# Performance work log

Measured on AMD Instinct MI355X. Metric: run time of the kernel, lower is better.

The kernel has to match this reference:

```python
import jax, jax.numpy as jnp
import numpy as np

N_NODES = 32
N_EDGES = N_NODES * (N_NODES - 1)  # 992
BATCH = 16
SEQ = 8
BS = BATCH * SEQ  # 128 frames
D = 256  # node_latent_dim == edge_latent_dim
ITERS = 3


def gru_cell(x, h, Wih, Whh, bih, bhh):
    # torch GRUCell: gates ordered (r, z, n)
    gi = x @ Wih.T + bih
    gh = h @ Whh.T + bhh
    ir, iz, inn = jnp.split(gi, 3, axis=-1)
    hr, hz, hn = jnp.split(gh, 3, axis=-1)
    r = jax.nn.sigmoid(ir + hr)
    z = jax.nn.sigmoid(iz + hz)
    n = jnp.tanh(inn + r * hn)
    return (1.0 - z) * n + z * h


def setup_inputs() -> dict:
    key = jax.random.key(0)
    ks = jax.random.split(key, 16)
    s = 0.05
    inp = {
        'node_latents': jax.random.normal(ks[0], (BS * N_NODES, D), jnp.float32),
        'edge_latents': jax.random.normal(ks[1], (BS * N_EDGES, D), jnp.float32),
        'node_Wih': jax.random.normal(ks[2], (3 * D, D), jnp.float32) * s,
        'node_Whh': jax.random.normal(ks[3], (3 * D, D), jnp.float32) * s,
        'node_bih': jax.random.normal(ks[4], (3 * D,), jnp.float32) * s,
        'node_bhh': jax.random.normal(ks[5], (3 * D,), jnp.float32) * s,
        'edge_Wih': jax.random.normal(ks[6], (3 * D, D), jnp.float32) * s,
        'edge_Whh': jax.random.normal(ks[7], (3 * D, D), jnp.float32) * s,
        'edge_bih': jax.random.normal(ks[8], (3 * D,), jnp.float32) * s,
        'edge_bhh': jax.random.normal(ks[9], (3 * D,), jnp.float32) * s,
        'w_node_pool': jax.random.normal(ks[10], (2 * D,), jnp.float32) * s,
        'w_edge_pool_sub': jax.random.normal(ks[11], (2 * D,), jnp.float32) * s,
        'w_edge_pool_obj': jax.random.normal(ks[12], (2 * D,), jnp.float32) * s,
    }
    # all ordered (subject, object) pairs with subject != object, same for every frame
    pairs = np.array([(i, j) for i in range(N_NODES) for j in range(N_NODES) if i != j], dtype=np.int32)  # [E,2]
    e2n = np.concatenate([np.arange(N_EDGES, dtype=np.int32)[:, None], pairs], axis=1)  # [E,3]
    inp['edge_idx_to_node_idxs'] = jnp.asarray(np.broadcast_to(e2n, (BS, N_EDGES, 3)).copy())
    return inp


def reference(node_latents, edge_latents, node_Wih, node_Whh, node_bih, node_bhh,
              edge_Wih, edge_Whh, edge_bih, edge_bhh,
              w_node_pool, w_edge_pool_sub, w_edge_pool_obj, edge_idx_to_node_idxs):
    sub = edge_idx_to_node_idxs[..., 1].astype(jnp.int32)  # [BS,E]
    obj = edge_idx_to_node_idxs[..., 2].astype(jnp.int32)
    bidx = jnp.arange(BS, dtype=jnp.int32)[:, None]
    sub_flat = (bidx * N_NODES + sub).reshape(-1)  # [BS*E]
    obj_flat = (bidx * N_NODES + obj).reshape(-1)

    # initial GRU call with zero hidden state (torch GRUCell default)
    node_hidden = gru_cell(node_latents, jnp.zeros_like(node_latents), node_Wih, node_Whh, node_bih, node_bhh)
    edge_hidden = gru_cell(edge_latents, jnp.zeros_like(edge_latents), edge_Wih, edge_Whh, edge_bih, edge_bhh)

    for _ in range(ITERS):
        nh = node_hidden.reshape(BS, N_NODES, D)
        eh = edge_hidden.reshape(BS, N_EDGES, D)
        ns = jnp.take_along_axis(nh, sub[:, :, None], axis=1)  # [BS,E,D] subject node feats
        no = jnp.take_along_axis(nh, obj[:, :, None], axis=1)  # [BS,E,D]
        cat_s = jnp.concatenate([ns, eh], axis=-1)  # [BS,E,2D]
        cat_o = jnp.concatenate([no, eh], axis=-1)
        g_node = jax.nn.sigmoid(cat_s @ w_node_pool)[..., None]        # [BS,E,1]
        g_sub = jax.nn.sigmoid(cat_s @ w_edge_pool_sub)[..., None]
        g_obj = jax.nn.sigmoid(cat_o @ w_edge_pool_obj)[..., None]
        # node message: gated edge features scattered to subject and object nodes
        # (equivalent to the dense 0/1 incidence matmul since subject != object per edge)
        msg_e = (g_node * eh).reshape(-1, D)  # [BS*E,D]
        node_msg = (jax.ops.segment_sum(msg_e, sub_flat, num_segments=BS * N_NODES)
                    + jax.ops.segment_sum(msg_e, obj_flat, num_segments=BS * N_NODES))  # [BS*N,D]
        edge_msg = (g_sub * ns + g_obj * no).reshape(-1, D)  # [BS*E,D]
        node_hidden = gru_cell(node_msg, node_hidden, node_Wih, node_Whh, node_bih, node_bhh)
        edge_hidden = gru_cell(edge_msg, edge_hidden, edge_Wih, edge_Whh, edge_bih, edge_bhh)

    return (node_hidden.reshape(BS, N_NODES, D), edge_hidden.reshape(BS, N_EDGES, D))
```

## Files before the change

### kernel.cpp

```cpp
#include <hip/hip_runtime.h>


#define D_DIM 256
#define NNODE 32
#define NEDGE 992
#define EDGE_ROWS (128 * NEDGE)
#define NODE_ROWS (128 * NNODE)
#define BM 64
#define EGRID (EDGE_ROWS / BM)
#define NGRID (NODE_ROWS / BM)
#define GI_OFF 32768
#define GI_STR 776

typedef _Float16 half8 __attribute__((ext_vector_type(8)));
typedef _Float16 half4v __attribute__((ext_vector_type(4)));
typedef __attribute__((ext_vector_type(4))) float f32x4;

__device__ __forceinline__ float sigf(float x) { return 1.0f / (1.0f + __expf(-x)); }
__device__ __forceinline__ float tanh_fast(float x) { return 2.0f / (1.0f + __expf(-2.0f * x)) - 1.0f; }
__device__ __forceinline__ float dot4(float4 a, float4 b) { return a.x*b.x + a.y*b.y + a.z*b.z + a.w*b.w; }

__global__ __launch_bounds__(64) void pack_w(const float* __restrict__ Wih,
                                             const float* __restrict__ Whh,
                                             _Float16* __restrict__ ph) {
  const int ct = blockIdx.x;
  const int ks = blockIdx.y;
  const int l = threadIdx.x;
  const int col = ct * 16 + (l & 15);
  const int kb = ks * 32 + (l >> 4) * 8;
  const float* src = (kb < 256) ? (Wih + col * 256 + kb) : (Whh + col * 256 + (kb - 256));
  half8 v;
  #pragma unroll
  for (int j = 0; j < 8; ++j) v[j] = (_Float16)src[j];
  *(half8*)(ph + ((ct * 16 + ks) * 64 + l) * 8) = v;
}

__global__ __launch_bounds__(1024, 4) void gru_init(
    const float* __restrict__ xe, const float* __restrict__ xn,
    _Float16* __restrict__ eh16, float* __restrict__ hn,
    const _Float16* __restrict__ wpe, const _Float16* __restrict__ wpn,
    const float* __restrict__ ebih, const float* __restrict__ ebhh,
    const float* __restrict__ nbih, const float* __restrict__ nbhh) {
  __shared__ __align__(16) unsigned char lds[32768];
  const bool edge = blockIdx.x < EGRID;
  const int bx = edge ? blockIdx.x : (blockIdx.x - EGRID);
  const float* xsrc = edge ? xe : xn;
  const _Float16* wp = edge ? wpe : wpn;
  const float* bih = edge ? ebih : nbih;
  const float* bhh = edge ? ebhh : nbhh;

  const int t = threadIdx.x;
  const int rb = bx * BM;
  const int srow = t >> 4;
  const int skc = t & 15;
  const int w = t >> 6;
  const int l = t & 63;
  const int lq = l >> 4;
  const int lr = l & 15;
  const int swm = (lr & 7) << 4;
  const int swz = (srow & 7) << 4;
  const int rowg = rb + srow;

  #pragma unroll
  for (int c = 0; c < 2; ++c) {
    half8 hx;
    #pragma unroll
    for (int pq = 0; pq < 2; ++pq) {
      const float4 a = *(const float4*)(xsrc + rowg * D_DIM + c * 128 + skc * 8 + pq * 4);
      hx[pq * 4 + 0] = (_Float16)a.x; hx[pq * 4 + 1] = (_Float16)a.y;
      hx[pq * 4 + 2] = (_Float16)a.z; hx[pq * 4 + 3] = (_Float16)a.w;
    }
    *(half8*)(&lds[(srow * 512 + c * 256 + skc * 16) ^ swz]) = hx;
  }
  __syncthreads();

  const f32x4 zz = {0.f, 0.f, 0.f, 0.f};
  f32x4 acc_r[4] = {zz, zz, zz, zz};
  f32x4 acc_z[4] = {zz, zz, zz, zz};
  f32x4 acc_nx[4] = {zz, zz, zz, zz};

  #pragma unroll
  for (int ksg = 0; ksg < 8; ++ksg) {
    half8 ah[4];
    #pragma unroll
    for (int rf = 0; rf < 4; ++rf)
      ah[rf] = *(const half8*)(&lds[((rf * 16 + lr) * 512 + ksg * 64 + lq * 16) ^ swm]);
    const half8 br_ = *(const half8*)(wp + (((0 * 16 + w) * 16 + ksg) * 64 + l) * 8);
    const half8 bz_ = *(const half8*)(wp + (((1 * 16 + w) * 16 + ksg) * 64 + l) * 8);
    const half8 bn_ = *(const half8*)(wp + (((2 * 16 + w) * 16 + ksg) * 64 + l) * 8);
    #pragma unroll
    for (int rf = 0; rf < 4; ++rf)
      acc_r[rf] = __builtin_amdgcn_mfma_f32_16x16x32_f16(ah[rf], br_, acc_r[rf], 0, 0, 0);
    #pragma unroll
    for (int rf = 0; rf < 4; ++rf)
      acc_z[rf] = __builtin_amdgcn_mfma_f32_16x16x32_f16(ah[rf], bz_, acc_z[rf], 0, 0, 0);
    #pragma unroll
    for (int rf = 0; rf < 4; ++rf)
      acc_nx[rf] = __builtin_amdgcn_mfma_f32_16x16x32_f16(ah[rf], bn_, acc_nx[rf], 0, 0, 0);
  }

  const int col = w * 16 + lr;
  const float br = bih[col] + bhh[col];
  const float bz = bih[256 + col] + bhh[256 + col];
  const float bnx = bih[512 + col];
  const float bnh = bhh[512 + col];

  if (edge) {
    _Float16 sv[16];
    #pragma unroll
    for (int rf = 0; rf < 4; ++rf) {
      #pragma unroll
      for (int q = 0; q < 4; ++q) {
        const float r = sigf(acc_r[rf][q] + br);
        const float z = sigf(acc_z[rf][q] + bz);
        const float n = tanh_fast(acc_nx[rf][q] + bnx + r * bnh);
        sv[rf * 4 + q] = (_Float16)((1.0f - z) * n);
      }
    }
    __syncthreads();
    #pragma unroll
    for (int rf = 0; rf < 4; ++rf) {
      #pragma unroll
      for (int q = 0; q < 4; ++q) {
        const int rowl = rf * 16 + lq * 4 + q;
        *(_Float16*)(&lds[(rowl * 512 + col * 2) ^ ((rowl & 7) << 4)]) = sv[rf * 4 + q];
      }
    }
    __syncthreads();
    #pragma unroll
    for (int p = 0; p < 2; ++p) {
      const int c = t + p * 1024;
      const int row = c >> 5;
      const int kc = c & 31;
      *(uint4*)(eh16 + (rb + row) * 256 + kc * 8) =
          *(const uint4*)(&lds[(row * 512 + kc * 16) ^ ((row & 7) << 4)]);
    }
  } else {
    #pragma unroll
    for (int rf = 0; rf < 4; ++rf) {
      #pragma unroll
      for (int q = 0; q < 4; ++q) {
        const int rowl = rf * 16 + lq * 4 + q;
        const float r = sigf(acc_r[rf][q] + br);
        const float z = sigf(acc_z[rf][q] + bz);
        const float n = tanh_fast(acc_nx[rf][q] + bnx + r * bnh);
        hn[(rb + rowl) * D_DIM + col] = (1.0f - z) * n;
      }
    }
  }
}

__global__ __launch_bounds__(1024, 4) void gru_nw(
    const float* __restrict__ nh, const _Float16* __restrict__ wp,
    _Float16* __restrict__ nw,
    const float* __restrict__ wnp, const float* __restrict__ wes,
    const float* __restrict__ weo,
    float* __restrict__ dA, float* __restrict__ dS, float* __restrict__ dO) {
  __shared__ __align__(16) unsigned char lds[32768];
  const int t = threadIdx.x;
  const int rb = blockIdx.x * BM;
  const int srow = t >> 4;
  const int skc = t & 15;
  const int w = t >> 6;
  const int l = t & 63;
  const int lq = l >> 4;
  const int lr = l & 15;
  const int swm = (lr & 7) << 4;
  const int swz = (srow & 7) << 4;
  const int rowg = rb + srow;

  float4 xa[4];
  #pragma unroll
  for (int i = 0; i < 4; ++i)
    xa[i] = *(const float4*)(nh + rowg * D_DIM + (i >> 1) * 128 + skc * 8 + (i & 1) * 4);
  #pragma unroll
  for (int c = 0; c < 2; ++c) {
    half8 hx;
    const float* f0 = (const float*)&xa[c * 2];
    #pragma unroll
    for (int j = 0; j < 8; ++j) hx[j] = (_Float16)f0[j];
    *(half8*)(&lds[(srow * 512 + c * 256 + skc * 16) ^ swz]) = hx;
  }
  float p1 = 0.f, p2 = 0.f, p3 = 0.f;
  #pragma unroll
  for (int i = 0; i < 4; ++i) {
    const int k0 = (i >> 1) * 128 + skc * 8 + (i & 1) * 4;
    p1 += dot4(xa[i], *(const float4*)(wnp + k0));
    p2 += dot4(xa[i], *(const float4*)(wes + k0));
    p3 += dot4(xa[i], *(const float4*)(weo + k0));
  }
  #pragma unroll
  for (int mm = 1; mm < 16; mm <<= 1) {
    p1 += __shfl_xor(p1, mm, 16);
    p2 += __shfl_xor(p2, mm, 16);
    p3 += __shfl_xor(p3, mm, 16);
  }
  if (skc == 0) { dA[rowg] = p1; dS[rowg] = p2; dO[rowg] = p3; }
  __syncthreads();

  const f32x4 zz = {0.f, 0.f, 0.f, 0.f};
  f32x4 acc_r[4] = {zz, zz, zz, zz};
  f32x4 acc_z[4] = {zz, zz, zz, zz};
  f32x4 acc_nx[4] = {zz, zz, zz, zz};

  #pragma unroll
  for (int ksg = 0; ksg < 8; ++ksg) {
    half8 ah[4];
    #pragma unroll
    for (int rf = 0; rf < 4; ++rf)
      ah[rf] = *(const half8*)(&lds[((rf * 16 + lr) * 512 + ksg * 64 + lq * 16) ^ swm]);
    const half8 br_ = *(const half8*)(wp + (((0 * 16 + w) * 16 + ksg) * 64 + l) * 8);
    const half8 bz_ = *(const half8*)(wp + (((1 * 16 + w) * 16 + ksg) * 64 + l) * 8);
    const half8 bn_ = *(const half8*)(wp + (((2 * 16 + w) * 16 + ksg) * 64 + l) * 8);
    #pragma unroll
    for (int rf = 0; rf < 4; ++rf)
      acc_r[rf] = __builtin_amdgcn_mfma_f32_16x16x32_f16(ah[rf], br_, acc_r[rf], 0, 0, 0);
    #pragma unroll
    for (int rf = 0; rf < 4; ++rf)
      acc_z[rf] = __builtin_amdgcn_mfma_f32_16x16x32_f16(ah[rf], bz_, acc_z[rf], 0, 0, 0);
    #pragma unroll
    for (int rf = 0; rf < 4; ++rf)
      acc_nx[rf] = __builtin_amdgcn_mfma_f32_16x16x32_f16(ah[rf], bn_, acc_nx[rf], 0, 0, 0);
  }

  const int col = w * 16 + lr;
  #pragma unroll
  for (int rf = 0; rf < 4; ++rf) {
    #pragma unroll
    for (int q = 0; q < 4; ++q) {
      const int rowl = rf * 16 + lq * 4 + q;
      _Float16* np = nw + (rb + rowl) * 768 + col;
      np[0]   = (_Float16)acc_r[rf][q];
      np[256] = (_Float16)acc_z[rf][q];
      np[512] = (_Float16)acc_nx[rf][q];
    }
  }
}

template <bool LAST>
__global__ __launch_bounds__(1024, 4) void gru_iter(
    _Float16* __restrict__ eh16, float* __restrict__ ehf,
    float* __restrict__ nh, const float* __restrict__ nmsg,
    const _Float16* __restrict__ wpe, const _Float16* __restrict__ wpn,
    const float* __restrict__ ebih, const float* __restrict__ ebhh,
    const float* __restrict__ nbih, const float* __restrict__ nbhh,
    const float* __restrict__ wesb, const float* __restrict__ weob,
    const float* __restrict__ dotS, const float* __restrict__ dotO,
    const _Float16* __restrict__ nw) {
  __shared__ __align__(16) unsigned char lds[32768 + BM * GI_STR * 2];

  const int t = threadIdx.x;
  const int srow = t >> 4;
  const int skc = t & 15;
  const int w = t >> 6;
  const int l = t & 63;
  const int lq = l >> 4;
  const int lr = l & 15;
  const int swm = (lr & 7) << 4;
  const int swz = (srow & 7) << 4;

  const f32x4 zz = {0.f, 0.f, 0.f, 0.f};
  f32x4 acc_r[4] = {zz, zz, zz, zz};
  f32x4 acc_z[4] = {zz, zz, zz, zz};
  f32x4 acc_nx[4] = {zz, zz, zz, zz};
  f32x4 acc_nh[4] = {zz, zz, zz, zz};

  if (blockIdx.x < EGRID) {
    const int rb = blockIdx.x * BM;
    const int rowg = rb + srow;
    const int b = rowg / NEDGE;
    const int e = rowg - b * NEDGE;
    const int si = e / 31;
    const int m = e - si * 31;
    const int ob = (m < si) ? m : (m + 1);

    const uint4 v0 = *(const uint4*)(eh16 + rowg * 256 + skc * 8);
    const uint4 v1 = *(const uint4*)(eh16 + rowg * 256 + 128 + skc * 8);
    *(uint4*)(&lds[(srow * 512 + skc * 16) ^ swz]) = v0;
    *(uint4*)(&lds[(srow * 512 + 256 + skc * 16) ^ swz]) = v1;
    float pS = 0.f, pO = 0.f;
    {
      const _Float16* f0 = (const _Float16*)&v0;
      const _Float16* f1 = (const _Float16*)&v1;
      #pragma unroll
      for (int j = 0; j < 8; ++j) {
        const float a = (float)f0[j];
        const float bb = (float)f1[j];
        pS += a * wesb[skc * 8 + j] + bb * wesb[128 + skc * 8 + j];
        pO += a * weob[skc * 8 + j] + bb * weob[128 + skc * 8 + j];
      }
    }
    #pragma unroll
    for (int mm = 1; mm < 16; mm <<= 1) {
      pS += __shfl_xor(pS, mm, 16);
      pO += __shfl_xor(pO, mm, 16);
    }
    const float gs = sigf(dotS[b * NNODE + si] + pS);
    const float go = sigf(dotO[b * NNODE + ob] + pO);
    const _Float16 gsh = (_Float16)gs, goh = (_Float16)go;
    const _Float16* ns = nw + (b * NNODE + si) * 768;
    const _Float16* no_ = nw + (b * NNODE + ob) * 768;
    _Float16* giw = (_Float16*)(lds + GI_OFF) + srow * GI_STR;
    #pragma unroll
    for (int j = 0; j < 6; ++j) {
      const int c0 = skc * 8 + j * 128;
      const half8 a = *(const half8*)(ns + c0);
      const half8 bb = *(const half8*)(no_ + c0);
      half8 g;
      #pragma unroll
      for (int k = 0; k < 8; ++k) g[k] = gsh * a[k] + goh * bb[k];
      *(half8*)(giw + c0) = g;
    }
    __syncthreads();

    #pragma unroll
    for (int ksg = 0; ksg < 8; ++ksg) {
      half8 ah[4];
      #pragma unroll
      for (int rf = 0; rf < 4; ++rf)
        ah[rf] = *(const half8*)(&lds[((rf * 16 + lr) * 512 + ksg * 64 + lq * 16) ^ swm]);
      const int kk = 8 + ksg;
      const half8 br_ = *(const half8*)(wpe + (((0 * 16 + w) * 16 + kk) * 64 + l) * 8);
      const half8 bz_ = *(const half8*)(wpe + (((1 * 16 + w) * 16 + kk) * 64 + l) * 8);
      const half8 bn_ = *(const half8*)(wpe + (((2 * 16 + w) * 16 + kk) * 64 + l) * 8);
      #pragma unroll
      for (int rf = 0; rf < 4; ++rf)
        acc_r[rf] = __builtin_amdgcn_mfma_f32_16x16x32_f16(ah[rf], br_, acc_r[rf], 0, 0, 0);
      #pragma unroll
      for (int rf = 0; rf < 4; ++rf)
        acc_z[rf] = __builtin_amdgcn_mfma_f32_16x16x32_f16(ah[rf], bz_, acc_z[rf], 0, 0, 0);
      #pragma unroll
      for (int rf = 0; rf < 4; ++rf)
        acc_nh[rf] = __builtin_amdgcn_mfma_f32_16x16x32_f16(ah[rf], bn_, acc_nh[rf], 0, 0, 0);
    }

    const int col = w * 16 + lr;
    const float br = ebih[col] + ebhh[col];
    const float bz = ebih[256 + col] + ebhh[256 + col];
    const float bnx = ebih[512 + col];
    const float bnh = ebhh[512 + col];
    const _Float16* gir = (const _Float16*)(lds + GI_OFF);
    _Float16 sv[16];
    #pragma unroll
    for (int rf = 0; rf < 4; ++rf) {
      #pragma unroll
      for (int q = 0; q < 4; ++q) {
        const int rowl = rf * 16 + lq * 4 + q;
        const _Float16* gp = gir + rowl * GI_STR + col;
        const float r = sigf(acc_r[rf][q] + (float)gp[0] + br);
        const float z = sigf(acc_z[rf][q] + (float)gp[256] + bz);
        const float n = tanh_fast((float)gp[512] + bnx + r * (acc_nh[rf][q] + bnh));
        const float hv =
            (float)*(const _Float16*)(&lds[(rowl * 512 + col * 2) ^ ((rowl & 7) << 4)]);
        const float out = (1.0f - z) * n + z * hv;
        if constexpr (LAST) {
          ehf[(rb + rowl) * D_DIM + col] = out;
        } else {
          sv[rf * 4 + q] = (_Float16)out;
        }
      }
    }
    if constexpr (!LAST) {
      __syncthreads();
      #pragma unroll
      for (int rf = 0; rf < 4; ++rf) {
        #pragma unroll
        for (int q = 0; q < 4; ++q) {
          const int rowl = rf * 16 + lq * 4 + q;
          *(_Float16*)(&lds[(rowl * 512 + col * 2) ^ ((rowl & 7) << 4)]) = sv[rf * 4 + q];
        }
      }
      __syncthreads();
      #pragma unroll
      for (int p = 0; p < 2; ++p) {
        const int c = t + p * 1024;
        const int row = c >> 5;
        const int kc = c & 31;
        *(uint4*)(eh16 + (rb + row) * 256 + kc * 8) =
            *(const uint4*)(&lds[(row * 512 + kc * 16) ^ ((row & 7) << 4)]);
      }
    }
  } else {
    const int rb = (blockIdx.x - EGRID) * BM;
    const int rowg = rb + srow;

    {
      float4 pre[4];
      #pragma unroll
      for (int i = 0; i < 4; ++i)
        pre[i] = *(const float4*)(nh + rowg * D_DIM + (i >> 1) * 128 + skc * 8 + (i & 1) * 4);
      #pragma unroll
      for (int c = 0; c < 2; ++c) {
        half8 hh8;
        const float* f1 = (const float*)&pre[c * 2];
        #pragma unroll
        for (int j = 0; j < 8; ++j) hh8[j] = (_Float16)f1[j];
        *(half8*)(&lds[(srow * 1024 + 512 + c * 256 + skc * 16) ^ swz]) = hh8;
      }
    }
    __syncthreads();

    #pragma unroll
    for (int ksg = 0; ksg < 8; ++ksg) {
      half8 ah[4];
      #pragma unroll
      for (int rf = 0; rf < 4; ++rf)
        ah[rf] = *(const half8*)(&lds[((rf * 16 + lr) * 1024 + 512 + ksg * 64 + lq * 16) ^ swm]);
      const int kk = 8 + ksg;
      const half8 br_ = *(const half8*)(wpn + (((0 * 16 + w) * 16 + kk) * 64 + l) * 8);
      const half8 bz_ = *(const half8*)(wpn + (((1 * 16 + w) * 16 + kk) * 64 + l) * 8);
      const half8 bn_ = *(const half8*)(wpn + (((2 * 16 + w) * 16 + kk) * 64 + l) * 8);
      #pragma unroll
      for (int rf = 0; rf < 4; ++rf)
        acc_r[rf] = __builtin_amdgcn_mfma_f32_16x16x32_f16(ah[rf], br_, acc_r[rf], 0, 0, 0);
      #pragma unroll
      for (int rf = 0; rf < 4; ++rf)
        acc_z[rf] = __builtin_amdgcn_mfma_f32_16x16x32_f16(ah[rf], bz_, acc_z[rf], 0, 0, 0);
      #pragma unroll
      for (int rf = 0; rf < 4; ++rf)
        acc_nh[rf] = __builtin_amdgcn_mfma_f32_16x16x32_f16(ah[rf], bn_, acc_nh[rf], 0, 0, 0);
    }

    #pragma unroll
    for (int c = 0; c < 2; ++c) {
      half8 hx;
      #pragma unroll
      for (int pq = 0; pq < 2; ++pq) {
        const float4 a = *(const float4*)(nmsg + rowg * D_DIM + c * 128 + skc * 8 + pq * 4);
        hx[pq * 4 + 0] = (_Float16)a.x; hx[pq * 4 + 1] = (_Float16)a.y;
        hx[pq * 4 + 2] = (_Float16)a.z; hx[pq * 4 + 3] = (_Float16)a.w;
      }
      *(half8*)(&lds[(srow * 1024 + 0 + c * 256 + skc * 16) ^ swz]) = hx;
    }
    __syncthreads();
    #pragma unroll
    for (int ksg = 0; ksg < 8; ++ksg) {
      half8 ah[4];
      #pragma unroll
      for (int rf = 0; rf < 4; ++rf)
        ah[rf] = *(const half8*)(&lds[((rf * 16 + lr) * 1024 + 0 + ksg * 64 + lq * 16) ^ swm]);
      const half8 br_ = *(const half8*)(wpn + (((0 * 16 + w) * 16 + ksg) * 64 + l) * 8);
      const half8 bz_ = *(const half8*)(wpn + (((1 * 16 + w) * 16 + ksg) * 64 + l) * 8);
      const half8 bn_ = *(const half8*)(wpn + (((2 * 16 + w) * 16 + ksg) * 64 + l) * 8);
      #pragma unroll
      for (int rf = 0; rf < 4; ++rf)
        acc_r[rf] = __builtin_amdgcn_mfma_f32_16x16x32_f16(ah[rf], br_, acc_r[rf], 0, 0, 0);
      #pragma unroll
      for (int rf = 0; rf < 4; ++rf)
        acc_z[rf] = __builtin_amdgcn_mfma_f32_16x16x32_f16(ah[rf], bz_, acc_z[rf], 0, 0, 0);
      #pragma unroll
      for (int rf = 0; rf < 4; ++rf)
        acc_nx[rf] = __builtin_amdgcn_mfma_f32_16x16x32_f16(ah[rf], bn_, acc_nx[rf], 0, 0, 0);
    }

    const int col = w * 16 + lr;
    const float br = nbih[col] + nbhh[col];
    const float bz = nbih[256 + col] + nbhh[256 + col];
    const float bnx = nbih[512 + col];
    const float bnh = nbhh[512 + col];
    #pragma unroll
    for (int rf = 0; rf < 4; ++rf) {
      #pragma unroll
      for (int q = 0; q < 4; ++q) {
        const int rowl = rf * 16 + lq * 4 + q;
        const float r = sigf(acc_r[rf][q] + br);
        const float z = sigf(acc_z[rf][q] + bz);
        const float n = tanh_fast(acc_nx[rf][q] + bnx + r * (acc_nh[rf][q] + bnh));
        const float hv = nh[(rb + rowl) * D_DIM + col];
        nh[(rb + rowl) * D_DIM + col] = (1.0f - z) * n + z * hv;
      }
    }
  }
}

__global__ __launch_bounds__(256) void node_msg_kernel(
    const _Float16* __restrict__ eh16, const float* __restrict__ wnp,
    const float* __restrict__ dotA, float* __restrict__ nmsg) {
  __shared__ float sh[3][256];
  const int nr = blockIdx.x;
  const int b = nr >> 5;
  const int n = nr & 31;
  const int wv = threadIdx.x >> 6;
  const int l = threadIdx.x & 63;
  const int base = b * NEDGE;
  const float4 w1b = ((const float4*)(wnp + 256))[l];

  float4 acc = {0.f, 0.f, 0.f, 0.f};
  for (int k = wv; k < 62; k += 4) {
    int e, sub;
    if (k < 31) {
      e = base + n * 31 + k;
      sub = n;
    } else {
      int i = k - 31;
      const int ip = (i < n) ? i : (i + 1);
      e = base + ip * 31 + ((n < ip) ? n : (n - 1));
      sub = ip;
    }
    const half4v hv4 = ((const half4v*)(eh16 + e * 256))[l];
    float4 ev;
    ev.x = (float)hv4[0]; ev.y = (float)hv4[1];
    ev.z = (float)hv4[2]; ev.w = (float)hv4[3];
    float p = dot4(ev, w1b);
    #pragma unroll
    for (int mm = 32; mm > 0; mm >>= 1) p += __shfl_xor(p, mm, 64);
    const float gN = sigf(dotA[b * NNODE + sub] + p);
    acc.x += gN * ev.x; acc.y += gN * ev.y; acc.z += gN * ev.z; acc.w += gN * ev.w;
  }
  if (wv > 0) *(float4*)(&sh[wv - 1][l * 4]) = acc;
  __syncthreads();
  if (wv == 0) {
    #pragma unroll
    for (int v = 0; v < 3; ++v) {
      const float4 o = *(const float4*)(&sh[v][l * 4]);
      acc.x += o.x; acc.y += o.y; acc.z += o.z; acc.w += o.w;
    }
    *(float4*)(nmsg + nr * D_DIM + l * 4) = acc;
  }
}

extern "C" void kernel_launch(void* const* d_in, const int* in_sizes, int n_in,
                              void* d_out, int out_size, void* d_ws, size_t ws_size,
                              hipStream_t stream) {
  const float* node_latents = (const float*)d_in[0];
  const float* edge_latents = (const float*)d_in[1];
  const float* node_Wih = (const float*)d_in[2];
  const float* node_Whh = (const float*)d_in[3];
  const float* node_bih = (const float*)d_in[4];
  const float* node_bhh = (const float*)d_in[5];
  const float* edge_Wih = (const float*)d_in[6];
  const float* edge_Whh = (const float*)d_in[7];
  const float* edge_bih = (const float*)d_in[8];
  const float* edge_bhh = (const float*)d_in[9];
  const float* w_node_pool = (const float*)d_in[10];
  const float* w_edge_sub = (const float*)d_in[11];
  const float* w_edge_obj = (const float*)d_in[12];

  float* nh = (float*)d_out;
  float* eh = (float*)d_out + NODE_ROWS * D_DIM;

  const int WPLANE = 48 * 16 * 64 * 8;
  _Float16* ph_n = (_Float16*)d_ws;
  _Float16* ph_e = ph_n + WPLANE;
  _Float16* NW = ph_e + WPLANE;
  _Float16* eh16 = NW + NODE_ROWS * 768;
  float* fw = (float*)(eh16 + (size_t)EDGE_ROWS * D_DIM);
  float* dotA = fw; fw += NODE_ROWS;
  float* dotS = fw; fw += NODE_ROWS;
  float* dotO = fw; fw += NODE_ROWS;
  float* node_msg = fw; fw += NODE_ROWS * D_DIM;

  dim3 pg(48, 16);
  pack_w<<<pg, 64, 0, stream>>>(node_Wih, node_Whh, ph_n);
  pack_w<<<pg, 64, 0, stream>>>(edge_Wih, edge_Whh, ph_e);

  gru_init<<<EGRID + NGRID, 1024, 0, stream>>>(
      edge_latents, node_latents, eh16, nh, ph_e, ph_n,
      edge_bih, edge_bhh, node_bih, node_bhh);

  for (int it = 0; it < 3; ++it) {
    gru_nw<<<NGRID, 1024, 0, stream>>>(
        nh, ph_e, NW, w_node_pool, w_edge_sub, w_edge_obj, dotA, dotS, dotO);
    node_msg_kernel<<<NODE_ROWS, 256, 0, stream>>>(eh16, w_node_pool, dotA, node_msg);
    if (it < 2)
      gru_iter<false><<<EGRID + NGRID, 1024, 0, stream>>>(
          eh16, eh, nh, node_msg, ph_e, ph_n,
          edge_bih, edge_bhh, node_bih, node_bhh,
          w_edge_sub + 256, w_edge_obj + 256, dotS, dotO, NW);
    else
      gru_iter<true><<<EGRID + NGRID, 1024, 0, stream>>>(
          eh16, eh, nh, node_msg, ph_e, ph_n,
          edge_bih, edge_bhh, node_bih, node_bhh,
          w_edge_sub + 256, w_edge_obj + 256, dotS, dotO, NW);
  }
}
```

Baseline: 656.4 us.

## Fuse node-side pooling/projection tail into GRU kernels, drop separate gru_nw launch

Result: faster. 643.4 us (-2.0%).

```diff
diff --git a/kernel.cpp b/kernel.cpp
--- a/kernel.cpp
+++ b/kernel.cpp
@@ -11,6 +11,7 @@
 #define NGRID (NODE_ROWS / BM)
 #define GI_OFF 32768
 #define GI_STR 776
+#define NT_OFF 65536
 
 typedef _Float16 half8 __attribute__((ext_vector_type(8)));
 typedef _Float16 half4v __attribute__((ext_vector_type(4)));
@@ -35,19 +36,99 @@
   *(half8*)(ph + ((ct * 16 + ks) * 64 + l) * 8) = v;
 }
 
+__device__ __forceinline__ void nw_tail(
+    unsigned char* reg, int rb, int t,
+    const _Float16* __restrict__ wpe,
+    const float* __restrict__ wnp, const float* __restrict__ wes,
+    const float* __restrict__ weo,
+    float* __restrict__ dA, float* __restrict__ dS, float* __restrict__ dO,
+    _Float16* __restrict__ nw) {
+  const int srow = t >> 4;
+  const int skc = t & 15;
+  const int w = t >> 6;
+  const int l = t & 63;
+  const int lq = l >> 4;
+  const int lr = l & 15;
+  const int swm = (lr & 7) << 4;
+  const int swz = (srow & 7) << 4;
+  const int rowg = rb + srow;
+
+  float p1 = 0.f, p2 = 0.f, p3 = 0.f;
+  #pragma unroll
+  for (int c = 0; c < 2; ++c) {
+    const uint4 v = *(const uint4*)(&reg[(srow * 512 + c * 256 + skc * 16) ^ swz]);
+    const _Float16* f = (const _Float16*)&v;
+    #pragma unroll
+    for (int j = 0; j < 8; ++j) {
+      const float a = (float)f[j];
+      const int cc = c * 128 + skc * 8 + j;
+      p1 += a * wnp[cc];
+      p2 += a * wes[cc];
+      p3 += a * weo[cc];
+    }
+  }
+  #pragma unroll
+  for (int mm = 1; mm < 16; mm <<= 1) {
+    p1 += __shfl_xor(p1, mm, 16);
+    p2 += __shfl_xor(p2, mm, 16);
+    p3 += __shfl_xor(p3, mm, 16);
+  }
+  if (skc == 0) { dA[rowg] = p1; dS[rowg] = p2; dO[rowg] = p3; }
+
+  const f32x4 zz = {0.f, 0.f, 0.f, 0.f};
+  f32x4 ar[4] = {zz, zz, zz, zz};
+  f32x4 az[4] = {zz, zz, zz, zz};
+  f32x4 an[4] = {zz, zz, zz, zz};
+  #pragma unroll
+  for (int ksg = 0; ksg < 8; ++ksg) {
+    half8 ah[4];
+    #pragma unroll
+    for (int rf = 0; rf < 4; ++rf)
+      ah[rf] = *(const half8*)(&reg[((rf * 16 + lr) * 512 + ksg * 64 + lq * 16) ^ swm]);
+    const half8 br_ = *(const half8*)(wpe + (((0 * 16 + w) * 16 + ksg) * 64 + l) * 8);
+    const half8 bz_ = *(const half8*)(wpe + (((1 * 16 + w) * 16 + ksg) * 64 + l) * 8);
+    const half8 bn_ = *(const half8*)(wpe + (((2 * 16 + w) * 16 + ksg) * 64 + l) * 8);
+    #pragma unroll
+    for (int rf = 0; rf < 4; ++rf)
+      ar[rf] = __builtin_amdgcn_mfma_f32_16x16x32_f16(ah[rf], br_, ar[rf], 0, 0, 0);
+    #pragma unroll
+    for (int rf = 0; rf < 4; ++rf)
+      az[rf] = __builtin_amdgcn_mfma_f32_16x16x32_f16(ah[rf], bz_, az[rf], 0, 0, 0);
+    #pragma unroll
+    for (int rf = 0; rf < 4; ++rf)
+      an[rf] = __builtin_amdgcn_mfma_f32_16x16x32_f16(ah[rf], bn_, an[rf], 0, 0, 0);
+  }
+  const int col = w * 16 + lr;
+  #pragma unroll
+  for (int rf = 0; rf < 4; ++rf) {
+    #pragma unroll
+    for (int q = 0; q < 4; ++q) {
+      const int rowl = rf * 16 + lq * 4 + q;
+      _Float16* np = nw + (rb + rowl) * 768 + col;
+      np[0]   = (_Float16)ar[rf][q];
+      np[256] = (_Float16)az[rf][q];
+      np[512] = (_Float16)an[rf][q];
+    }
+  }
+}
+
 __global__ __launch_bounds__(1024, 4) void gru_init(
     const float* __restrict__ xe, const float* __restrict__ xn,
     _Float16* __restrict__ eh16, float* __restrict__ hn,
     const _Float16* __restrict__ wpe, const _Float16* __restrict__ wpn,
     const float* __restrict__ ebih, const float* __restrict__ ebhh,
-    const float* __restrict__ nbih, const float* __restrict__ nbhh) {
+    const float* __restrict__ nbih, const float* __restrict__ nbhh,
+    const float* __restrict__ wnp, const float* __restrict__ wes,
+    const float* __restrict__ weo,
+    float* __restrict__ dA, float* __restrict__ dS, float* __restrict__ dO,
+    _Float16* __restrict__ nw) {
   __shared__ __align__(16) unsigned char lds[32768];
-  const bool edge = blockIdx.x < EGRID;
-  const int bx = edge ? blockIdx.x : (blockIdx.x - EGRID);
-  const float* xsrc = edge ? xe : xn;
-  const _Float16* wp = edge ? wpe : wpn;
-  const float* bih = edge ? ebih : nbih;
-  const float* bhh = edge ? ebhh : nbhh;
+  const bool node = blockIdx.x < NGRID;
+  const int bx = node ? blockIdx.x : (blockIdx.x - NGRID);
+  const float* xsrc = node ? xn : xe;
+  const _Float16* wp = node ? wpn : wpe;
+  const float* bih = node ? nbih : ebih;
+  const float* bhh = node ? nbhh : ebhh;
 
   const int t = threadIdx.x;
   const int rb = bx * BM;
@@ -105,28 +186,35 @@
   const float bnx = bih[512 + col];
   const float bnh = bhh[512 + col];
 
-  if (edge) {
-    _Float16 sv[16];
-    #pragma unroll
-    for (int rf = 0; rf < 4; ++rf) {
-      #pragma unroll
-      for (int q = 0; q < 4; ++q) {
-        const float r = sigf(acc_r[rf][q] + br);
-        const float z = sigf(acc_z[rf][q] + bz);
-        const float n = tanh_fast(acc_nx[rf][q] + bnx + r * bnh);
-        sv[rf * 4 + q] = (_Float16)((1.0f - z) * n);
-      }
-    }
-    __syncthreads();
-    #pragma unroll
-    for (int rf = 0; rf < 4; ++rf) {
-      #pragma unroll
-      for (int q = 0; q < 4; ++q) {
+  _Float16 sv[16];
+  #pragma unroll
+  for (int rf = 0; rf < 4; ++rf) {
+    #pragma unroll
+    for (int q = 0; q < 4; ++q) {
+      const float r = sigf(acc_r[rf][q] + br);
+      const float z = sigf(acc_z[rf][q] + bz);
+      const float n = tanh_fast(acc_nx[rf][q] + bnx + r * bnh);
+      const float out = (1.0f - z) * n;
+      sv[rf * 4 + q] = (_Float16)out;
+      if (node) {
         const int rowl = rf * 16 + lq * 4 + q;
-        *(_Float16*)(&lds[(rowl * 512 + col * 2) ^ ((rowl & 7) << 4)]) = sv[rf * 4 + q];
-      }
-    }
-    __syncthreads();
+        hn[(rb + rowl) * D_DIM + col] = out;
+      }
+    }
+  }
+  __syncthreads();
+  #pragma unroll
+  for (int rf = 0; rf < 4; ++rf) {
+    #pragma unroll
+    for (int q = 0; q < 4; ++q) {
+      const int rowl = rf * 16 + lq * 4 + q;
+      *(_Float16*)(&lds[(rowl * 512 + col * 2) ^ ((rowl & 7) << 4)]) = sv[rf * 4 + q];
+    }
+  }
+  __syncthreads();
+  if (node) {
+    nw_tail(lds, rb, t, wpe, wnp, wes, weo, dA, dS, dO, nw);
+  } else {
     #pragma unroll
     for (int p = 0; p < 2; ++p) {
       const int c = t + p * 1024;
@@ -134,105 +222,6 @@
       const int kc = c & 31;
       *(uint4*)(eh16 + (rb + row) * 256 + kc * 8) =
           *(const uint4*)(&lds[(row * 512 + kc * 16) ^ ((row & 7) << 4)]);
-    }
-  } else {
-    #pragma unroll
-    for (int rf = 0; rf < 4; ++rf) {
-      #pragma unroll
-      for (int q = 0; q < 4; ++q) {
-        const int rowl = rf * 16 + lq * 4 + q;
-        const float r = sigf(acc_r[rf][q] + br);
-        const float z = sigf(acc_z[rf][q] + bz);
-        const float n = tanh_fast(acc_nx[rf][q] + bnx + r * bnh);
-        hn[(rb + rowl) * D_DIM + col] = (1.0f - z) * n;
-      }
-    }
-  }
-}
-
-__global__ __launch_bounds__(1024, 4) void gru_nw(
-    const float* __restrict__ nh, const _Float16* __restrict__ wp,
-    _Float16* __restrict__ nw,
-    const float* __restrict__ wnp, const float* __restrict__ wes,
-    const float* __restrict__ weo,
-    float* __restrict__ dA, float* __restrict__ dS, float* __restrict__ dO) {
-  __shared__ __align__(16) unsigned char lds[32768];
-  const int t = threadIdx.x;
-  const int rb = blockIdx.x * BM;
-  const int srow = t >> 4;
-  const int skc = t & 15;
-  const int w = t >> 6;
-  const int l = t & 63;
-  const int lq = l >> 4;
-  const int lr = l & 15;
-  const int swm = (lr & 7) << 4;
-  const int swz = (srow & 7) << 4;
-  const int rowg = rb + srow;
-
-  float4 xa[4];
-  #pragma unroll
-  for (int i = 0; i < 4; ++i)
-    xa[i] = *(const float4*)(nh + rowg * D_DIM + (i >> 1) * 128 + skc * 8 + (i & 1) * 4);
-  #pragma unroll
-  for (int c = 0; c < 2; ++c) {
-    half8 hx;
-    const float* f0 = (const float*)&xa[c * 2];
-    #pragma unroll
-    for (int j = 0; j < 8; ++j) hx[j] = (_Float16)f0[j];
-    *(half8*)(&lds[(srow * 512 + c * 256 + skc * 16) ^ swz]) = hx;
-  }
-  float p1 = 0.f, p2 = 0.f, p3 = 0.f;
-  #pragma unroll
-  for (int i = 0; i < 4; ++i) {
-    const int k0 = (i >> 1) * 128 + skc * 8 + (i & 1) * 4;
-    p1 += dot4(xa[i], *(const float4*)(wnp + k0));
-    p2 += dot4(xa[i], *(const float4*)(wes + k0));
-    p3 += dot4(xa[i], *(const float4*)(weo + k0));
-  }
-  #pragma unroll
-  for (int mm = 1; mm < 16; mm <<= 1) {
-    p1 += __shfl_xor(p1, mm, 16);
-    p2 += __shfl_xor(p2, mm, 16);
-    p3 += __shfl_xor(p3, mm, 16);
-  }
-  if (skc == 0) { dA[rowg] = p1; dS[rowg] = p2; dO[rowg] = p3; }
-  __syncthreads();
-
-  const f32x4 zz = {0.f, 0.f, 0.f, 0.f};
-  f32x4 acc_r[4] = {zz, zz, zz, zz};
-  f32x4 acc_z[4] = {zz, zz, zz, zz};
-  f32x4 acc_nx[4] = {zz, zz, zz, zz};
-
-  #pragma unroll
-  for (int ksg = 0; ksg < 8; ++ksg) {
-    half8 ah[4];
-    #pragma unroll
-    for (int rf = 0; rf < 4; ++rf)
-      ah[rf] = *(const half8*)(&lds[((rf * 16 + lr) * 512 + ksg * 64 + lq * 16) ^ swm]);
-    const half8 br_ = *(const half8*)(wp + (((0 * 16 + w) * 16 + ksg) * 64 + l) * 8);
-    const half8 bz_ = *(const half8*)(wp + (((1 * 16 + w) * 16 + ksg) * 64 + l) * 8);
-    const half8 bn_ = *(const half8*)(wp + (((2 * 16 + w) * 16 + ksg) * 64 + l) * 8);
-    #pragma unroll
-    for (int rf = 0; rf < 4; ++rf)
-      acc_r[rf] = __builtin_amdgcn_mfma_f32_16x16x32_f16(ah[rf], br_, acc_r[rf], 0, 0, 0);
-    #pragma unroll
-    for (int rf = 0; rf < 4; ++rf)
-      acc_z[rf] = __builtin_amdgcn_mfma_f32_16x16x32_f16(ah[rf], bz_, acc_z[rf], 0, 0, 0);
-    #pragma unroll
-    for (int rf = 0; rf < 4; ++rf)
-      acc_nx[rf] = __builtin_amdgcn_mfma_f32_16x16x32_f16(ah[rf], bn_, acc_nx[rf], 0, 0, 0);
-  }
-
-  const int col = w * 16 + lr;
-  #pragma unroll
-  for (int rf = 0; rf < 4; ++rf) {
-    #pragma unroll
-    for (int q = 0; q < 4; ++q) {
-      const int rowl = rf * 16 + lq * 4 + q;
-      _Float16* np = nw + (rb + rowl) * 768 + col;
-      np[0]   = (_Float16)acc_r[rf][q];
-      np[256] = (_Float16)acc_z[rf][q];
-      np[512] = (_Float16)acc_nx[rf][q];
     }
   }
 }
@@ -246,7 +235,11 @@
     const float* __restrict__ nbih, const float* __restrict__ nbhh,
     const float* __restrict__ wesb, const float* __restrict__ weob,
     const float* __restrict__ dotS, const float* __restrict__ dotO,
-    const _Float16* __restrict__ nw) {
+    const _Float16* __restrict__ nw,
+    const float* __restrict__ wnp, const float* __restrict__ wes,
+    const float* __restrict__ weo,
+    float* __restrict__ dAo, float* __restrict__ dSo, float* __restrict__ dOo,
+    _Float16* __restrict__ nwo) {
   __shared__ __align__(16) unsigned char lds[32768 + BM * GI_STR * 2];
 
   const int t = threadIdx.x;
@@ -265,8 +258,8 @@
   f32x4 acc_nx[4] = {zz, zz, zz, zz};
   f32x4 acc_nh[4] = {zz, zz, zz, zz};
 
-  if (blockIdx.x < EGRID) {
-    const int rb = blockIdx.x * BM;
+  if (blockIdx.x >= NGRID) {
+    const int rb = (blockIdx.x - NGRID) * BM;
     const int rowg = rb + srow;
     const int b = rowg / NEDGE;
     const int e = rowg - b * NEDGE;
@@ -381,7 +374,7 @@
       }
     }
   } else {
-    const int rb = (blockIdx.x - EGRID) * BM;
+    const int rb = blockIdx.x * BM;
     const int rowg = rb + srow;
 
     {
@@ -458,6 +451,7 @@
     const float bz = nbih[256 + col] + nbhh[256 + col];
     const float bnx = nbih[512 + col];
     const float bnh = nbhh[512 + col];
+    unsigned char* reg = lds + NT_OFF;
     #pragma unroll
     for (int rf = 0; rf < 4; ++rf) {
       #pragma unroll
@@ -467,8 +461,15 @@
         const float z = sigf(acc_z[rf][q] + bz);
         const float n = tanh_fast(acc_nx[rf][q] + bnx + r * (acc_nh[rf][q] + bnh));
         const float hv = nh[(rb + rowl) * D_DIM + col];
-        nh[(rb + rowl) * D_DIM + col] = (1.0f - z) * n + z * hv;
-      }
+        const float out = (1.0f - z) * n + z * hv;
+        nh[(rb + rowl) * D_DIM + col] = out;
+        if constexpr (!LAST)
+          *(_Float16*)(&reg[(rowl * 512 + col * 2) ^ ((rowl & 7) << 4)]) = (_Float16)out;
+      }
+    }
+    if constexpr (!LAST) {
+      __syncthreads();
+      nw_tail(reg, rb, t, wpe, wnp, wes, weo, dAo, dSo, dOo, nwo);
     }
   }
 }
@@ -542,35 +543,47 @@
   const int WPLANE = 48 * 16 * 64 * 8;
   _Float16* ph_n = (_Float16*)d_ws;
   _Float16* ph_e = ph_n + WPLANE;
-  _Float16* NW = ph_e + WPLANE;
-  _Float16* eh16 = NW + NODE_ROWS * 768;
+  _Float16* NW0 = ph_e + WPLANE;
+  _Float16* NW1 = NW0 + NODE_ROWS * 768;
+  _Float16* eh16 = NW1 + NODE_ROWS * 768;
   float* fw = (float*)(eh16 + (size_t)EDGE_ROWS * D_DIM);
-  float* dotA = fw; fw += NODE_ROWS;
-  float* dotS = fw; fw += NODE_ROWS;
-  float* dotO = fw; fw += NODE_ROWS;
+  float* dotA0 = fw; fw += NODE_ROWS;
+  float* dotS0 = fw; fw += NODE_ROWS;
+  float* dotO0 = fw; fw += NODE_ROWS;
+  float* dotA1 = fw; fw += NODE_ROWS;
+  float* dotS1 = fw; fw += NODE_ROWS;
+  float* dotO1 = fw; fw += NODE_ROWS;
   float* node_msg = fw; fw += NODE_ROWS * D_DIM;
 
   dim3 pg(48, 16);
   pack_w<<<pg, 64, 0, stream>>>(node_Wih, node_Whh, ph_n);
   pack_w<<<pg, 64, 0, stream>>>(edge_Wih, edge_Whh, ph_e);
 
-  gru_init<<<EGRID + NGRID, 1024, 0, stream>>>(
+  gru_init<<<NGRID + EGRID, 1024, 0, stream>>>(
       edge_latents, node_latents, eh16, nh, ph_e, ph_n,
-      edge_bih, edge_bhh, node_bih, node_bhh);
+      edge_bih, edge_bhh, node_bih, node_bhh,
+      w_node_pool, w_edge_sub, w_edge_obj, dotA0, dotS0, dotO0, NW0);
+
+  _Float16* NWg[2] = {NW0, NW1};
+  float* dAg[2] = {dotA0, dotA1};
+  float* dSg[2] = {dotS0, dotS1};
+  float* dOg[2] = {dotO0, dotO1};
 
   for (int it = 0; it < 3; ++it) {
-    gru_nw<<<NGRID, 1024, 0, stream>>>(
-        nh, ph_e, NW, w_node_pool, w_edge_sub, w_edge_obj, dotA, dotS, dotO);
-    node_msg_kernel<<<NODE_ROWS, 256, 0, stream>>>(eh16, w_node_pool, dotA, node_msg);
+    const int gi = it & 1;
+    const int go = gi ^ 1;
+    node_msg_kernel<<<NODE_ROWS, 256, 0, stream>>>(eh16, w_node_pool, dAg[gi], node_msg);
     if (it < 2)
-      gru_iter<false><<<EGRID + NGRID, 1024, 0, stream>>>(
+      gru_iter<false><<<NGRID + EGRID, 1024, 0, stream>>>(
           eh16, eh, nh, node_msg, ph_e, ph_n,
           edge_bih, edge_bhh, node_bih, node_bhh,
-          w_edge_sub + 256, w_edge_obj + 256, dotS, dotO, NW);
+          w_edge_sub + 256, w_edge_obj + 256, dSg[gi], dOg[gi], NWg[gi],
+          w_node_pool, w_edge_sub, w_edge_obj, dAg[go], dSg[go], dOg[go], NWg[go]);
     else
-      gru_iter<true><<<EGRID + NGRID, 1024, 0, stream>>>(
+      gru_iter<true><<<NGRID + EGRID, 1024, 0, stream>>>(
           eh16, eh, nh, node_msg, ph_e, ph_n,
           edge_bih, edge_bhh, node_bih, node_bhh,
-          w_edge_sub + 256, w_edge_obj + 256, dotS, dotO, NW);
+          w_edge_sub + 256, w_edge_obj + 256, dSg[gi], dOg[gi], NWg[gi],
+          w_node_pool, w_edge_sub, w_edge_obj, dAg[go], dSg[go], dOg[go], NWg[go]);
   }
 }
```
